# Performance work log

Measured on AMD Instinct MI355X. Metric: run time of the kernel, lower is better.

## Reference

```python
import jax, jax.numpy as jnp
import numpy as np

B, E, H, W = 8, 1024, 16, 1024
DH = E // H


def setup_inputs() -> dict:
    key = jax.random.key(0)
    ks = jax.random.split(key, 5)
    scale = E ** (-0.5)
    return {
        "x": jax.random.normal(ks[0], (3, B, E, W), dtype=jnp.float32),
        "L_Q": jax.random.normal(ks[1], (E, E), dtype=jnp.float32) * scale,
        "L_K": jax.random.normal(ks[2], (E, E), dtype=jnp.float32) * scale,
        "L_V": jax.random.normal(ks[3], (E, E), dtype=jnp.float32) * scale,
        "dense_M": jax.random.normal(ks[4], (E, E), dtype=jnp.float32) * scale,
        "dense_b": jnp.zeros((E, 1), dtype=jnp.float32),
    }


def reference(x, L_Q, L_K, L_V, dense_M, dense_b):
    # x: [3, B, E, W], channels-first sequences (dropout layers are identity in eval)
    K, Q, V = x[0], x[1], x[2]                      # each [B, E, W]
    K = jnp.einsum('ef,bfw->bew', L_K, K)
    Q = jnp.einsum('ef,bfw->bew', L_Q, Q)
    V = jnp.einsum('ef,bfw->bew', L_V, V)
    Kv = K.reshape(B, H, DH, W)
    Qv = Q.reshape(B, H, DH, W)
    Vv = V.reshape(B, H, DH, W)
    # Q_v^T @ K_v -> [B, H, Wq, Wk]
    scores = jnp.einsum('bhdq,bhdk->bhqk', Qv, Kv)
    # causal_factor = tril(-inf, diag=-1): -inf strictly below the diagonal (q > k)
    qi = jnp.arange(W)[:, None]
    ki = jnp.arange(W)[None, :]
    scores = jnp.where(qi > ki, -jnp.inf, scores)
    # softmax over the QUERY axis (-2), post-scaled by E^-0.5 (non-standard)
    attn = jax.nn.softmax(scores, axis=-2) * (E ** (-0.5))
    # V_v @ scores: contract over the query axis -> [B, H, DH, Wk]
    out = jnp.einsum('bhdq,bhqk->bhdk', Vv, attn).reshape(B, E, W)
    # dense output projection: M @ out + b (bias broadcasts over W)
    return jnp.einsum('ef,bfw->bew', dense_M, out) + dense_b
```

## Files before the change

kernel.cpp:

```cpp
#include <hip/hip_runtime.h>

typedef float  f4  __attribute__((ext_vector_type(4)));
typedef short  s8v __attribute__((ext_vector_type(8)));
typedef unsigned short u16;
typedef u16 us4 __attribute__((ext_vector_type(4)));

constexpr int En  = 1024;
constexpr int Wn  = 1024;
constexpr int Bn  = 8;
constexpr int Hn  = 16;
constexpr int DHn = 64;

__device__ inline u16 bf16rn(float x) {
    unsigned u = __float_as_uint(x);
    return (u16)((u + 0x7FFFu + ((u >> 16) & 1u)) >> 16);
}
__device__ inline float bf16tof(u16 h) { return __uint_as_float(((unsigned)h) << 16); }

#define GLD_LDS16(gp, lp) __builtin_amdgcn_global_load_lds(                      \
    (const __attribute__((address_space(1))) void*)(gp),                         \
    (__attribute__((address_space(3))) void*)(lp), 16, 0, 0)

__global__ void split_plain(const float* __restrict__ in, u16* __restrict__ hi,
                            u16* __restrict__ lo, int n4) {
    int i = blockIdx.x * blockDim.x + threadIdx.x;
    if (i >= n4) return;
    f4 v = ((const f4*)in)[i];
    us4 h, l;
    #pragma unroll
    for (int k = 0; k < 4; ++k) {
        u16 hh = bf16rn(v[k]);
        h[k] = hh;
        l[k] = bf16rn(v[k] - bf16tof(hh));
    }
    ((us4*)hi)[i] = h;
    ((us4*)lo)[i] = l;
}

__global__ __launch_bounds__(256)
void split_t(const float* __restrict__ in, u16* __restrict__ hi,
             u16* __restrict__ lo) {
    __shared__ float T[32][33];
    const int z = blockIdx.z;
    const size_t zo = (size_t)z * En * Wn;
    const int r0 = blockIdx.y * 32, c0 = blockIdx.x * 32;
    const int t = threadIdx.x;
    const int row = t >> 3, c4 = (t & 7) << 2;

    f4 v = *(const f4*)&in[zo + (size_t)(r0 + row) * Wn + c0 + c4];
    T[row][c4 + 0] = v[0]; T[row][c4 + 1] = v[1];
    T[row][c4 + 2] = v[2]; T[row][c4 + 3] = v[3];
    __syncthreads();

    const int oc = row, r4 = c4;
    us4 h, l;
    #pragma unroll
    for (int i = 0; i < 4; ++i) {
        float x = T[r4 + i][oc];
        u16 hh = bf16rn(x);
        h[i] = hh;
        l[i] = bf16rn(x - bf16tof(hh));
    }
    *(us4*)&hi[zo + (size_t)(c0 + oc) * En + r0 + r4] = h;
    *(us4*)&lo[zo + (size_t)(c0 + oc) * En + r0 + r4] = l;
}

template<int MODE>
__global__ __launch_bounds__(256, 2)
void gemm_mfma(const u16* __restrict__ Ah,  const u16* __restrict__ Al,
               const u16* __restrict__ Bth, const u16* __restrict__ Btl,
               float* __restrict__ Yf, u16* __restrict__ Yh, u16* __restrict__ Yl,
               const float* __restrict__ bias) {
    __shared__ u16 AsH[4096], AsL[4096], BsH[4096], BsL[4096];

    const int z  = blockIdx.z;
    const size_t zB = (size_t)z * Wn * En;
    const int e0 = blockIdx.y * 128, n0 = blockIdx.x * 128;
    const int t = threadIdx.x, lane = t & 63, wave = t >> 6;
    const int q = lane >> 4, r = lane & 15;
    const int m_off = (wave & 1) * 64, n_off = (wave >> 1) * 64;

    f4 acc[4][4];
    #pragma unroll
    for (int i = 0; i < 4; ++i)
        #pragma unroll
        for (int j = 0; j < 4; ++j) { acc[i][j][0]=0; acc[i][j][1]=0; acc[i][j][2]=0; acc[i][j][3]=0; }

    for (int kb = 0; kb < En; kb += 32) {
        __syncthreads();
        #pragma unroll
        for (int it = 0; it < 2; ++it) {
            const int id = t + 256 * it;
            const int u = id >> 3;
            const int p = (id & 7) ^ (u & 7);
            const int m = 2 * u + (p >> 2), g = p & 3;
            const size_t colA = (size_t)kb + 8 * g;
            const u16* ga_h = Ah  + (size_t)(e0 + m) * En + colA;
            const u16* ga_l = Al  + (size_t)(e0 + m) * En + colA;
            const u16* gb_h = Bth + zB + (size_t)(n0 + m) * En + colA;
            const u16* gb_l = Btl + zB + (size_t)(n0 + m) * En + colA;
            GLD_LDS16(ga_h, &AsH[id * 8]);
            GLD_LDS16(ga_l, &AsL[id * 8]);
            GLD_LDS16(gb_h, &BsH[id * 8]);
            GLD_LDS16(gb_l, &BsL[id * 8]);
        }
        __syncthreads();

        s8v aH[4], aL[4], bH[4], bL[4];
        #pragma unroll
        for (int i = 0; i < 4; ++i) {
            const int Ra = m_off + 16 * i + r;
            const int Rb = n_off + 16 * i + r;
            const int sa = ((((Ra & 1) << 2) | q) ^ ((Ra >> 1) & 7));
            const int sb = ((((Rb & 1) << 2) | q) ^ ((Rb >> 1) & 7));
            const int ai = ((Ra >> 1) * 8 + sa) * 8;
            const int bi = ((Rb >> 1) * 8 + sb) * 8;
            aH[i] = *(const s8v*)&AsH[ai];
            aL[i] = *(const s8v*)&AsL[ai];
            bH[i] = *(const s8v*)&BsH[bi];
            bL[i] = *(const s8v*)&BsL[bi];
        }
        #pragma unroll
        for (int i = 0; i < 4; ++i)
            #pragma unroll
            for (int j = 0; j < 4; ++j) {
                acc[i][j] = __builtin_amdgcn_mfma_f32_16x16x32_bf16(aH[i], bH[j], acc[i][j], 0, 0, 0);
                acc[i][j] = __builtin_amdgcn_mfma_f32_16x16x32_bf16(aH[i], bL[j], acc[i][j], 0, 0, 0);
                acc[i][j] = __builtin_amdgcn_mfma_f32_16x16x32_bf16(aL[i], bH[j], acc[i][j], 0, 0, 0);
            }
    }

    if constexpr (MODE == 0) {
        const size_t zY = (size_t)z * En * Wn;
        #pragma unroll
        for (int i = 0; i < 4; ++i) {
            #pragma unroll
            for (int reg = 0; reg < 4; ++reg) {
                const int e = e0 + m_off + 16 * i + q * 4 + reg;
                const float bv = bias ? bias[e] : 0.0f;
                #pragma unroll
                for (int j = 0; j < 4; ++j) {
                    const int w = n0 + n_off + 16 * j + r;
                    Yf[zY + (size_t)e * Wn + w] = acc[i][j][reg] + bv;
                }
            }
        }
    }
    if constexpr (MODE == 1) {
        #pragma unroll
        for (int i = 0; i < 4; ++i) {
            const int e_base = e0 + m_off + 16 * i + q * 4;
            const int bh_e = z * Hn + (e_base >> 6);
            const int d0 = e_base & 63;
            #pragma unroll
            for (int j = 0; j < 4; ++j) {
                const int w = n0 + n_off + 16 * j + r;
                us4 h, l;
                #pragma unroll
                for (int reg = 0; reg < 4; ++reg) {
                    float x = acc[i][j][reg];
                    u16 hh = bf16rn(x);
                    h[reg] = hh;
                    l[reg] = bf16rn(x - bf16tof(hh));
                }
                const size_t o = ((size_t)bh_e * Wn + w) * 64 + d0;
                *(us4*)&Yh[o] = h;
                *(us4*)&Yl[o] = l;
            }
        }
    }
    if constexpr (MODE == 2) {
        #pragma unroll
        for (int i = 0; i < 4; ++i) {
            #pragma unroll
            for (int reg = 0; reg < 4; ++reg) {
                const int e = e0 + m_off + 16 * i + q * 4 + reg;
                const int bh_e = z * Hn + (e >> 6);
                const int d = e & 63;
                const size_t ro = ((size_t)bh_e * 64 + d) * Wn;
                #pragma unroll
                for (int j = 0; j < 4; ++j) {
                    const int w = n0 + n_off + 16 * j + r;
                    Yh[ro + w] = bf16rn(acc[i][j][reg]);
                }
            }
        }
    }
}

__global__ __launch_bounds__(256, 3)
void attn_mfma3(const u16* __restrict__ QTh, const u16* __restrict__ QTl,
                const u16* __restrict__ KTh, const u16* __restrict__ KTl,
                const u16* __restrict__ Vb,  u16* __restrict__ AoTh,
                u16* __restrict__ AoTl) {
    __shared__ u16 QsH[4096], QsL[4096], Vs[4096];
    __shared__ u16 PT[4][16][72];

    const int id   = blockIdx.x;
    const int rest = id >> 3;
    const int kb   = 15 - (rest & 15);
    const int bh   = (id & 7) + 8 * (rest >> 4);

    const int t = threadIdx.x, lane = t & 63, wave = t >> 6;
    const int r = lane & 15, quad = lane >> 4;
    const int k0 = kb * 64;
    const int kcol = k0 + wave * 16 + r;
    u16 (*pt)[72] = PT[wave];

    const size_t qkb = (size_t)bh * Wn * 64;
    const size_t vbb = (size_t)bh * 64 * Wn;

    s8v kH[2], kL[2];
    #pragma unroll
    for (int s = 0; s < 2; ++s) {
        const size_t a = qkb + (size_t)kcol * 64 + s * 32 + quad * 8;
        kH[s] = *(const s8v*)&KTh[a];
        kL[s] = *(const s8v*)&KTl[a];
    }

    f4 o[4];
    #pragma unroll
    for (int i = 0; i < 4; ++i) { o[i][0]=0; o[i][1]=0; o[i][2]=0; o[i][3]=0; }
    float m = -1e30f, l = 0.0f;

    const int c0 = t,       row0 = c0 >> 3, p0 = (c0 & 7) ^ (row0 & 7);
    const int c1 = t + 256, row1 = c1 >> 3, p1 = (c1 & 7) ^ (row1 & 7);

    s8v Aqh0, Aqh1, Aql0, Aql1, Av0, Av1;
    s8v Bqh0, Bqh1, Bql0, Bql1, Bv0, Bv1;

    auto ld = [&](int q0, s8v& qh0, s8v& qh1, s8v& ql0, s8v& ql1,
                  s8v& v0, s8v& v1) {
        const size_t g = qkb + (size_t)q0 * 64;
        qh0 = *(const s8v*)&QTh[g + (size_t)row0 * 64 + p0 * 8];
        ql0 = *(const s8v*)&QTl[g + (size_t)row0 * 64 + p0 * 8];
        v0  = *(const s8v*)&Vb[vbb + (size_t)row0 * Wn + q0 + p0 * 8];
        qh1 = *(const s8v*)&QTh[g + (size_t)row1 * 64 + p1 * 8];
        ql1 = *(const s8v*)&QTl[g + (size_t)row1 * 64 + p1 * 8];
        v1  = *(const s8v*)&Vb[vbb + (size_t)row1 * Wn + q0 + p1 * 8];
    };
    auto wr = [&](s8v& qh0, s8v& qh1, s8v& ql0, s8v& ql1, s8v& v0, s8v& v1) {
        *(s8v*)&QsH[c0 * 8] = qh0; *(s8v*)&QsL[c0 * 8] = ql0; *(s8v*)&Vs[c0 * 8] = v0;
        *(s8v*)&QsH[c1 * 8] = qh1; *(s8v*)&QsL[c1 * 8] = ql1; *(s8v*)&Vs[c1 * 8] = v1;
    };

    auto compute = [&](int q0) {
        f4 sacc[4];
        #pragma unroll
        for (int mt = 0; mt < 4; ++mt) { sacc[mt][0]=0; sacc[mt][1]=0; sacc[mt][2]=0; sacc[mt][3]=0; }
        #pragma unroll
        for (int s = 0; s < 2; ++s) {
            const int sw = (((s * 4 + quad) ^ (r & 7)) << 3);
            #pragma unroll
            for (int mt = 0; mt < 4; ++mt) {
                const int a = (16 * mt + r) * 64 + sw;
                s8v qh = *(const s8v*)&QsH[a];
                s8v ql = *(const s8v*)&QsL[a];
                sacc[mt] = __builtin_amdgcn_mfma_f32_16x16x32_bf16(qh, kH[s], sacc[mt], 0, 0, 0);
                sacc[mt] = __builtin_amdgcn_mfma_f32_16x16x32_bf16(qh, kL[s], sacc[mt], 0, 0, 0);
                sacc[mt] = __builtin_amdgcn_mfma_f32_16x16x32_bf16(ql, kH[s], sacc[mt], 0, 0, 0);
            }
        }
        if (q0 == k0) {
            const int klocal = wave * 16 + r;
            #pragma unroll
            for (int mt = 0; mt < 4; ++mt)
                #pragma unroll
                for (int reg = 0; reg < 4; ++reg)
                    if (16 * mt + quad * 4 + reg > klocal) sacc[mt][reg] = -1e30f;
        }
        float tm = -1e30f;
        #pragma unroll
        for (int mt = 0; mt < 4; ++mt)
            #pragma unroll
            for (int reg = 0; reg < 4; ++reg) tm = fmaxf(tm, sacc[mt][reg]);
        tm = fmaxf(tm, __shfl_xor(tm, 16));
        tm = fmaxf(tm, __shfl_xor(tm, 32));
        const float mnew  = fmaxf(m, tm);
        const float alpha = __expf(m - mnew);
        float ps = 0.0f;
        #pragma unroll
        for (int mt = 0; mt < 4; ++mt) {
            us4 pk;
            #pragma unroll
            for (int reg = 0; reg < 4; ++reg) {
                float p = __expf(sacc[mt][reg] - mnew);
                ps += p;
                pk[reg] = bf16rn(p);
            }
            *(us4*)&pt[r][16 * mt + quad * 4] = pk;
        }
        ps += __shfl_xor(ps, 16);
        ps += __shfl_xor(ps, 32);
        l = l * alpha + ps;
        m = mnew;
        #pragma unroll
        for (int i = 0; i < 4; ++i) {
            o[i][0] *= alpha; o[i][1] *= alpha; o[i][2] *= alpha; o[i][3] *= alpha;
        }
        #pragma unroll
        for (int s = 0; s < 2; ++s) {
            const int sw = (((s * 4 + quad) ^ (r & 7)) << 3);
            s8v pf = *(const s8v*)&pt[r][s * 32 + quad * 8];
            #pragma unroll
            for (int i = 0; i < 4; ++i) {
                s8v vf = *(const s8v*)&Vs[(16 * i + r) * 64 + sw];
                o[i] = __builtin_amdgcn_mfma_f32_16x16x32_bf16(vf, pf, o[i], 0, 0, 0);
            }
        }
    };

    ld(0, Aqh0, Aqh1, Aql0, Aql1, Av0, Av1);
    int q0 = 0;
    for (;;) {
        __syncthreads();
        wr(Aqh0, Aqh1, Aql0, Aql1, Av0, Av1);
        __syncthreads();
        if (q0 + 64 <= k0) ld(q0 + 64, Bqh0, Bqh1, Bql0, Bql1, Bv0, Bv1);
        compute(q0);
        q0 += 64;
        if (q0 > k0) break;
        __syncthreads();
        wr(Bqh0, Bqh1, Bql0, Bql1, Bv0, Bv1);
        __syncthreads();
        if (q0 + 64 <= k0) ld(q0 + 64, Aqh0, Aqh1, Aql0, Aql1, Av0, Av1);
        compute(q0);
        q0 += 64;
        if (q0 > k0) break;
    }

    const float inv = 1.0f / (l * 32.0f);
    const size_t ob0 = (size_t)(bh >> 4) * ((size_t)Wn * En) +
                       (size_t)kcol * En + (bh & 15) * 64 + quad * 4;
    #pragma unroll
    for (int i = 0; i < 4; ++i) {
        us4 h, lo4;
        #pragma unroll
        for (int reg = 0; reg < 4; ++reg) {
            float x = o[i][reg] * inv;
            u16 hh = bf16rn(x);
            h[reg] = hh;
            lo4[reg] = bf16rn(x - bf16tof(hh));
        }
        *(us4*)&AoTh[ob0 + 16 * i] = h;
        *(us4*)&AoTl[ob0 + 16 * i] = lo4;
    }
}

__global__ __launch_bounds__(256, 2)
void gemm128(const float* __restrict__ L, const float* __restrict__ X,
             float* __restrict__ Y, const float* __restrict__ bias) {
    __shared__ float As[16][132];
    __shared__ float Bs[16][132];

    const int bz = blockIdx.z;
    const float* Xb = X + (size_t)bz * En * Wn;
    float*       Yb = Y + (size_t)bz * En * Wn;
    const int e0 = blockIdx.y * 128;
    const int w0 = blockIdx.x * 128;
    const int t  = threadIdx.x;
    const int tx = t & 15, ty = t >> 4;
    const int la_e = t >> 2, la_f = (t & 3) << 2;
    const int lb_f = t >> 5, lb_w = (t & 31) << 2;

    float acc[2][2][4][4] = {};

    for (int f0 = 0; f0 < En; f0 += 16) {
        f4 a0 = *(const f4*)&L [(size_t)(e0 + la_e)      * En + f0 + la_f];
        f4 a1 = *(const f4*)&L [(size_t)(e0 + la_e + 64) * En + f0 + la_f];
        f4 b0 = *(const f4*)&Xb[(size_t)(f0 + lb_f)      * Wn + w0 + lb_w];
        f4 b1 = *(const f4*)&Xb[(size_t)(f0 + lb_f + 8)  * Wn + w0 + lb_w];
        __syncthreads();
        As[la_f + 0][la_e] = a0[0]; As[la_f + 1][la_e] = a0[1];
        As[la_f + 2][la_e] = a0[2]; As[la_f + 3][la_e] = a0[3];
        As[la_f + 0][la_e + 64] = a1[0]; As[la_f + 1][la_e + 64] = a1[1];
        As[la_f + 2][la_e + 64] = a1[2]; As[la_f + 3][la_e + 64] = a1[3];
        *(f4*)&Bs[lb_f    ][lb_w] = b0;
        *(f4*)&Bs[lb_f + 8][lb_w] = b1;
        __syncthreads();
        #pragma unroll
        for (int kk = 0; kk < 16; ++kk) {
            f4 av0 = *(f4*)&As[kk][ty * 4];
            f4 av1 = *(f4*)&As[kk][ty * 4 + 64];
            f4 bv0 = *(f4*)&Bs[kk][tx * 4];
            f4 bv1 = *(f4*)&Bs[kk][tx * 4 + 64];
            #pragma unroll
            for (int i = 0; i < 4; ++i)
                #pragma unroll
                for (int j = 0; j < 4; ++j) {
                    acc[0][0][i][j] = fmaf(av0[i], bv0[j], acc[0][0][i][j]);
                    acc[0][1][i][j] = fmaf(av0[i], bv1[j], acc[0][1][i][j]);
                    acc[1][0][i][j] = fmaf(av1[i], bv0[j], acc[1][0][i][j]);
                    acc[1][1][i][j] = fmaf(av1[i], bv1[j], acc[1][1][i][j]);
                }
        }
    }

    #pragma unroll
    for (int eh = 0; eh < 2; ++eh)
        #pragma unroll
        for (int i = 0; i < 4; ++i) {
            const int e = e0 + eh * 64 + ty * 4 + i;
            const float bv = bias ? bias[e] : 0.0f;
            #pragma unroll
            for (int wh = 0; wh < 2; ++wh) {
                f4 v;
                #pragma unroll
                for (int j = 0; j < 4; ++j) v[j] = acc[eh][wh][i][j] + bv;
                *(f4*)&Yb[(size_t)e * Wn + w0 + wh * 64 + tx * 4] = v;
            }
        }
}

__global__ __launch_bounds__(256, 2)
void attn64(const float* __restrict__ Qg, const float* __restrict__ Kg,
            const float* __restrict__ Vg, float* __restrict__ Og) {
    __shared__ float Ks[64][68];
    __shared__ float QP[64][68];
    __shared__ float Vt[64][68];
    __shared__ float mArr[64], lArr[64], alphaArr[64];
    __shared__ float red[4][64];

    const int kb = blockIdx.x, h = blockIdx.y, b = blockIdx.z;
    const size_t base = ((size_t)b * En + (size_t)h * DHn) * Wn;
    const float* Qp = Qg + base;
    const float* Kp = Kg + base;
    const float* Vp = Vg + base;
    float*       Op = Og + base;

    const int t  = threadIdx.x;
    const int tx = t & 15, ty = t >> 4;
    const int lr = t >> 4;
    const int lc = (t & 15) << 2;
    const int k0 = kb * 64;
    const int kc = t & 63, qg = t >> 6;

    #pragma unroll
    for (int r = 0; r < 4; ++r)
        *(f4*)&Ks[lr + r * 16][lc] =
            *(const f4*)&Kp[(size_t)(lr + r * 16) * Wn + k0 + lc];
    if (t < 64) { mArr[t] = -1e30f; lArr[t] = 0.0f; }
    float acc[4][4] = {};
    __syncthreads();

    for (int q0 = 0; q0 <= k0; q0 += 64) {
        #pragma unroll
        for (int r = 0; r < 4; ++r) {
            const int d = lr + r * 16;
            f4 qv = *(const f4*)&Qp[(size_t)d * Wn + q0 + lc];
            f4 vv = *(const f4*)&Vp[(size_t)d * Wn + q0 + lc];
            *(f4*)&QP[d][lc] = qv;
            Vt[lc + 0][d] = vv[0]; Vt[lc + 1][d] = vv[1];
            Vt[lc + 2][d] = vv[2]; Vt[lc + 3][d] = vv[3];
        }
        __syncthreads();

        float s[4][4] = {};
        #pragma unroll 4
        for (int d = 0; d < 64; ++d) {
            f4 kv = *(f4*)&Ks[d][tx * 4];
            f4 q2 = *(f4*)&QP[d][ty * 4];
            #pragma unroll
            for (int i = 0; i < 4; ++i)
                #pragma unroll
                for (int j = 0; j < 4; ++j)
                    s[i][j] = fmaf(q2[i], kv[j], s[i][j]);
        }
        if (q0 == k0) {
            #pragma unroll
            for (int i = 0; i < 4; ++i)
                #pragma unroll
                for (int j = 0; j < 4; ++j)
                    if (ty * 4 + i > tx * 4 + j) s[i][j] = -1e30f;
        }
        __syncthreads();
        #pragma unroll
        for (int i = 0; i < 4; ++i) {
            f4 v;
            #pragma unroll
            for (int j = 0; j < 4; ++j) v[j] = s[i][j];
            *(f4*)&QP[ty * 4 + i][tx * 4] = v;
        }
        __syncthreads();

        float sv[16];
        float lm = -1e30f;
        #pragma unroll
        for (int r = 0; r < 16; ++r) {
            sv[r] = QP[qg * 16 + r][kc];
            lm = fmaxf(lm, sv[r]);
        }
        red[qg][kc] = lm;
        __syncthreads();
        const float mt    = fmaxf(fmaxf(red[0][kc], red[1][kc]),
                                  fmaxf(red[2][kc], red[3][kc]));
        const float mprev = mArr[kc];
        const float mnew  = fmaxf(mprev, mt);
        float psum = 0.0f;
        #pragma unroll
        for (int r = 0; r < 16; ++r) {
            const float p = __expf(sv[r] - mnew);
            psum += p;
            QP[qg * 16 + r][kc] = p;
        }
        __syncthreads();
        red[qg][kc] = psum;
        __syncthreads();
        if (qg == 0) {
            const float alpha = __expf(mprev - mnew);
            lArr[kc] = lArr[kc] * alpha +
                       (red[0][kc] + red[1][kc] + red[2][kc] + red[3][kc]);
            mArr[kc]     = mnew;
            alphaArr[kc] = alpha;
        }
        __syncthreads();

        f4 al = *(f4*)&alphaArr[tx * 4];
        #pragma unroll
        for (int i = 0; i < 4; ++i)
            #pragma unroll
            for (int j = 0; j < 4; ++j)
                acc[i][j] *= al[j];
        #pragma unroll 4
        for (int q = 0; q < 64; ++q) {
            f4 pv = *(f4*)&QP[q][tx * 4];
            f4 v2 = *(f4*)&Vt[q][ty * 4];
            #pragma unroll
            for (int i = 0; i < 4; ++i)
                #pragma unroll
                for (int j = 0; j < 4; ++j)
                    acc[i][j] = fmaf(v2[i], pv[j], acc[i][j]);
        }
        __syncthreads();
    }

    f4 linv = *(f4*)&lArr[tx * 4];
    #pragma unroll
    for (int j = 0; j < 4; ++j) linv[j] = 1.0f / (linv[j] * 32.0f);
    #pragma unroll
    for (int i = 0; i < 4; ++i) {
        f4 v;
        #pragma unroll
        for (int j = 0; j < 4; ++j) v[j] = acc[i][j] * linv[j];
        *(f4*)&Op[(size_t)(ty * 4 + i) * Wn + k0 + tx * 4] = v;
    }
}

extern "C" void kernel_launch(void* const* d_in, const int* in_sizes, int n_in,
                              void* d_out, int out_size, void* d_ws, size_t ws_size,
                              hipStream_t stream) {
    const float* x    = (const float*)d_in[0];
    const float* L_Q  = (const float*)d_in[1];
    const float* L_K  = (const float*)d_in[2];
    const float* L_V  = (const float*)d_in[3];
    const float* M    = (const float*)d_in[4];
    const float* bias = (const float*)d_in[5];
    float* out = (float*)d_out;

    const size_t mat   = (size_t)Bn * En * Wn;
    const size_t matB  = mat * 4;
    const size_t lmatB = (size_t)En * En * 2;
    const size_t need  = 8 * lmatB + 4 * matB + matB / 2 + matB;

    if (ws_size >= need) {
        char* w = (char*)d_ws;
        u16*  Lsp = (u16*)w;
        char* XT  = w + 8 * lmatB;
        char* R1  = XT + matB;
        char* R2  = R1 + matB;
        char* R3  = R2 + matB;
        char* R4  = R3 + matB / 2;

        u16* LKh = Lsp + 0 * (lmatB / 2); u16* LKl = Lsp + 1 * (lmatB / 2);
        u16* LQh = Lsp + 2 * (lmatB / 2); u16* LQl = Lsp + 3 * (lmatB / 2);
        u16* LVh = Lsp + 4 * (lmatB / 2); u16* LVl = Lsp + 5 * (lmatB / 2);
        u16* Mh  = Lsp + 6 * (lmatB / 2); u16* Ml  = Lsp + 7 * (lmatB / 2);

        u16* XT_H = (u16*)XT;  u16* XT_L = (u16*)(XT + matB / 2);
        u16* KT_h = (u16*)R1;  u16* KT_l = (u16*)(R1 + matB / 2);
        u16* QT_h = (u16*)R2;  u16* QT_l = (u16*)(R2 + matB / 2);
        u16* Vb   = (u16*)R3;
        u16* AoTh = (u16*)R4;  u16* AoTl = (u16*)(R4 + matB / 2);

        const int n4L = En * En / 4;
        hipLaunchKernelGGL(split_plain, dim3(n4L / 256), dim3(256), 0, stream, L_K, LKh, LKl, n4L);
        hipLaunchKernelGGL(split_plain, dim3(n4L / 256), dim3(256), 0, stream, L_Q, LQh, LQl, n4L);
        hipLaunchKernelGGL(split_plain, dim3(n4L / 256), dim3(256), 0, stream, L_V, LVh, LVl, n4L);
        hipLaunchKernelGGL(split_plain, dim3(n4L / 256), dim3(256), 0, stream, M,   Mh,  Ml,  n4L);

        dim3 gt(Wn / 32, En / 32, Bn), bt(256);
        dim3 gg(Wn / 128, En / 128, Bn), bg(256);

        hipLaunchKernelGGL(split_t, gt, bt, 0, stream, x + 0 * mat, XT_H, XT_L);
        hipLaunchKernelGGL(HIP_KERNEL_NAME(gemm_mfma<1>), gg, bg, 0, stream,
                           LKh, LKl, XT_H, XT_L, (float*)nullptr, KT_h, KT_l, (const float*)nullptr);
        hipLaunchKernelGGL(split_t, gt, bt, 0, stream, x + 1 * mat, XT_H, XT_L);
        hipLaunchKernelGGL(HIP_KERNEL_NAME(gemm_mfma<1>), gg, bg, 0, stream,
                           LQh, LQl, XT_H, XT_L, (float*)nullptr, QT_h, QT_l, (const float*)nullptr);
        hipLaunchKernelGGL(split_t, gt, bt, 0, stream, x + 2 * mat, XT_H, XT_L);
        hipLaunchKernelGGL(HIP_KERNEL_NAME(gemm_mfma<2>), gg, bg, 0, stream,
                           LVh, LVl, XT_H, XT_L, (float*)nullptr, Vb, (u16*)nullptr, (const float*)nullptr);

        hipLaunchKernelGGL(attn_mfma3, dim3(2048), dim3(256), 0, stream,
                           QT_h, QT_l, KT_h, KT_l, Vb, AoTh, AoTl);

        hipLaunchKernelGGL(HIP_KERNEL_NAME(gemm_mfma<0>), gg, bg, 0, stream,
                           Mh, Ml, AoTh, AoTl, out, (u16*)nullptr, (u16*)nullptr, bias);
    } else {
        float* ws = (float*)d_ws;
        float* Kp = ws;
        float* Qp = ws + mat;
        float* Vp = ws + 2 * mat;
        float* Ao = ws + 3 * mat;

        dim3 gg(Wn / 128, En / 128, Bn), blk(256);
        hipLaunchKernelGGL(gemm128, gg, blk, 0, stream, L_K, x + 0 * mat, Kp, (const float*)nullptr);
        hipLaunchKernelGGL(gemm128, gg, blk, 0, stream, L_Q, x + 1 * mat, Qp, (const float*)nullptr);
        hipLaunchKernelGGL(gemm128, gg, blk, 0, stream, L_V, x + 2 * mat, Vp, (const float*)nullptr);

        dim3 ga(Wn / 64, Hn, Bn);
        hipLaunchKernelGGL(attn64, ga, blk, 0, stream, Qp, Kp, Vp, Ao);

        hipLaunchKernelGGL(gemm128, gg, blk, 0, stream, M, Ao, out, bias);
    }
}
```

Baseline: 465.4 us.

## Batch weight splits, stream B fragments, raise occupancy, prioritize MFMA waves

Merges the four weight hi/lo split launches into one kernel launch indexed by blockIdx.y. In the GEMM, B fragments are now loaded per column tile inside the MFMA loop rather than all up front, which cuts register pressure; the launch bound is raised to 3 blocks per CU. The attention kernel raises its occupancy hint to 4 and wraps the MFMA sections in s_setprio so waves issuing matrix math get priority. Higher occupancy targets may force register spills, and streaming the B loads can expose LDS latency.

```diff
diff --git a/kernel.cpp b/kernel.cpp
--- a/kernel.cpp
+++ b/kernel.cpp
@@ -21,10 +21,16 @@
     (const __attribute__((address_space(1))) void*)(gp),                         \
     (__attribute__((address_space(3))) void*)(lp), 16, 0, 0)
 
-__global__ void split_plain(const float* __restrict__ in, u16* __restrict__ hi,
-                            u16* __restrict__ lo, int n4) {
+__global__ void split_plain4(const float* __restrict__ p0,
+                             const float* __restrict__ p1,
+                             const float* __restrict__ p2,
+                             const float* __restrict__ p3,
+                             u16* __restrict__ base) {
+    const int z = blockIdx.y;
+    const float* in = (z == 0) ? p0 : (z == 1) ? p1 : (z == 2) ? p2 : p3;
+    u16* hi = base + (size_t)(2 * z) * En * En;
+    u16* lo = base + (size_t)(2 * z + 1) * En * En;
     int i = blockIdx.x * blockDim.x + threadIdx.x;
-    if (i >= n4) return;
     f4 v = ((const f4*)in)[i];
     us4 h, l;
     #pragma unroll
@@ -66,7 +72,7 @@
 }
 
 template<int MODE>
-__global__ __launch_bounds__(256, 2)
+__global__ __launch_bounds__(256, 3)
 void gemm_mfma(const u16* __restrict__ Ah,  const u16* __restrict__ Al,
                const u16* __restrict__ Bth, const u16* __restrict__ Btl,
                float* __restrict__ Yf, u16* __restrict__ Yh, u16* __restrict__ Yl,
@@ -106,28 +112,29 @@
         }
         __syncthreads();
 
-        s8v aH[4], aL[4], bH[4], bL[4];
+        s8v aH[4], aL[4];
         #pragma unroll
         for (int i = 0; i < 4; ++i) {
             const int Ra = m_off + 16 * i + r;
-            const int Rb = n_off + 16 * i + r;
             const int sa = ((((Ra & 1) << 2) | q) ^ ((Ra >> 1) & 7));
-            const int sb = ((((Rb & 1) << 2) | q) ^ ((Rb >> 1) & 7));
             const int ai = ((Ra >> 1) * 8 + sa) * 8;
-            const int bi = ((Rb >> 1) * 8 + sb) * 8;
             aH[i] = *(const s8v*)&AsH[ai];
             aL[i] = *(const s8v*)&AsL[ai];
-            bH[i] = *(const s8v*)&BsH[bi];
-            bL[i] = *(const s8v*)&BsL[bi];
-        }
-        #pragma unroll
-        for (int i = 0; i < 4; ++i)
-            #pragma unroll
-            for (int j = 0; j < 4; ++j) {
-                acc[i][j] = __builtin_amdgcn_mfma_f32_16x16x32_bf16(aH[i], bH[j], acc[i][j], 0, 0, 0);
-                acc[i][j] = __builtin_amdgcn_mfma_f32_16x16x32_bf16(aH[i], bL[j], acc[i][j], 0, 0, 0);
-                acc[i][j] = __builtin_amdgcn_mfma_f32_16x16x32_bf16(aL[i], bH[j], acc[i][j], 0, 0, 0);
-            }
+        }
+        #pragma unroll
+        for (int j = 0; j < 4; ++j) {
+            const int Rb = n_off + 16 * j + r;
+            const int sb = ((((Rb & 1) << 2) | q) ^ ((Rb >> 1) & 7));
+            const int bi = ((Rb >> 1) * 8 + sb) * 8;
+            s8v bH = *(const s8v*)&BsH[bi];
+            s8v bL = *(const s8v*)&BsL[bi];
+            #pragma unroll
+            for (int i = 0; i < 4; ++i) {
+                acc[i][j] = __builtin_amdgcn_mfma_f32_16x16x32_bf16(aH[i], bH, acc[i][j], 0, 0, 0);
+                acc[i][j] = __builtin_amdgcn_mfma_f32_16x16x32_bf16(aH[i], bL, acc[i][j], 0, 0, 0);
+                acc[i][j] = __builtin_amdgcn_mfma_f32_16x16x32_bf16(aL[i], bH, acc[i][j], 0, 0, 0);
+            }
+        }
     }
 
     if constexpr (MODE == 0) {
@@ -188,7 +195,7 @@
     }
 }
 
-__global__ __launch_bounds__(256, 3)
+__global__ __launch_bounds__(256, 4)
 void attn_mfma3(const u16* __restrict__ QTh, const u16* __restrict__ QTl,
                 const u16* __restrict__ KTh, const u16* __restrict__ KTl,
                 const u16* __restrict__ Vb,  u16* __restrict__ AoTh,
@@ -248,6 +255,7 @@
         f4 sacc[4];
         #pragma unroll
         for (int mt = 0; mt < 4; ++mt) { sacc[mt][0]=0; sacc[mt][1]=0; sacc[mt][2]=0; sacc[mt][3]=0; }
+        __builtin_amdgcn_s_setprio(1);
         #pragma unroll
         for (int s = 0; s < 2; ++s) {
             const int sw = (((s * 4 + quad) ^ (r & 7)) << 3);
@@ -261,6 +269,7 @@
                 sacc[mt] = __builtin_amdgcn_mfma_f32_16x16x32_bf16(ql, kH[s], sacc[mt], 0, 0, 0);
             }
         }
+        __builtin_amdgcn_s_setprio(0);
         if (q0 == k0) {
             const int klocal = wave * 16 + r;
             #pragma unroll
@@ -298,6 +307,7 @@
         for (int i = 0; i < 4; ++i) {
             o[i][0] *= alpha; o[i][1] *= alpha; o[i][2] *= alpha; o[i][3] *= alpha;
         }
+        __builtin_amdgcn_s_setprio(1);
         #pragma unroll
         for (int s = 0; s < 2; ++s) {
             const int sw = (((s * 4 + quad) ^ (r & 7)) << 3);
@@ -308,6 +318,7 @@
                 o[i] = __builtin_amdgcn_mfma_f32_16x16x32_bf16(vf, pf, o[i], 0, 0, 0);
             }
         }
+        __builtin_amdgcn_s_setprio(0);
     };
 
     ld(0, Aqh0, Aqh1, Aql0, Aql1, Av0, Av1);
@@ -583,10 +594,8 @@
         u16* AoTh = (u16*)R4;  u16* AoTl = (u16*)(R4 + matB / 2);
 
         const int n4L = En * En / 4;
-        hipLaunchKernelGGL(split_plain, dim3(n4L / 256), dim3(256), 0, stream, L_K, LKh, LKl, n4L);
-        hipLaunchKernelGGL(split_plain, dim3(n4L / 256), dim3(256), 0, stream, L_Q, LQh, LQl, n4L);
-        hipLaunchKernelGGL(split_plain, dim3(n4L / 256), dim3(256), 0, stream, L_V, LVh, LVl, n4L);
-        hipLaunchKernelGGL(split_plain, dim3(n4L / 256), dim3(256), 0, stream, M,   Mh,  Ml,  n4L);
+        hipLaunchKernelGGL(split_plain4, dim3(n4L / 256, 4), dim3(256), 0, stream,
+                           L_K, L_Q, L_V, M, Lsp);
 
         dim3 gt(Wn / 32, En / 32, Bn), bt(256);
         dim3 gg(Wn / 128, En / 128, Bn), bg(256);
```

After: 491.8 us. +5.7%, slower.
